# Kernel tuning notes

Hardware: AMD Instinct MI355X
Metric: run time of the kernel (lower is better)

The kernel has to match this reference:

```python
import jax, jax.numpy as jnp
import numpy as np

D, H, COND, MLP_RATIO = 1024, 16, 1024, 4
HD = D // H
DFF = MLP_RATIO * D


def layer_norm(x, w, eps=1e-5):
    xf = x.astype(jnp.float32)
    mu = jnp.mean(xf, axis=-1, keepdims=True)
    var = jnp.mean((xf - mu) ** 2, axis=-1, keepdims=True)
    return (xf - mu) * jax.lax.rsqrt(var + eps) * w


def rms_norm(x, w, eps=1e-6):
    xf = x.astype(jnp.float32)
    rms = jnp.sqrt(jnp.mean(xf * xf, axis=-1, keepdims=True) + eps)
    return (xf / rms * w).astype(x.dtype)


def rotate_half(x):
    x1, x2 = x[..., : x.shape[-1] // 2], x[..., x.shape[-1] // 2:]
    return jnp.concatenate([-x2, x1], axis=-1)


def apply_rope(x, cos, sin):
    return x * cos + rotate_half(x) * sin


def setup_inputs() -> dict:
    key = jax.random.key(0)
    ks = jax.random.split(key, 16)
    B, S = 4, 2048
    pos = jnp.arange(S, dtype=jnp.float32)
    inv = 1.0 / (10000.0 ** (jnp.arange(0, HD, 2, dtype=jnp.float32) / HD))
    freqs = pos[:, None] * inv[None, :]              # (S, HD/2)
    emb = jnp.concatenate([freqs, freqs], axis=-1)   # (S, HD)
    return {
        "x": jax.random.normal(ks[0], (B, S, D), jnp.float32),
        "cos": jnp.cos(emb)[None, :, None, :],        # (1,S,1,HD)
        "sin": jnp.sin(emb)[None, :, None, :],
        "c": jax.random.normal(ks[1], (B, COND), jnp.float32),
        "norm1_w": jnp.ones((D,), jnp.float32),
        "Wqkv": jax.random.normal(ks[2], (D, 3 * D), jnp.float32) * 0.02,
        "Wout": jax.random.normal(ks[3], (D, D), jnp.float32) * 0.02,
        "q_norm_w": jnp.ones((HD,), jnp.float32),
        "k_norm_w": jnp.ones((HD,), jnp.float32),
        "norm2_w": jnp.ones((D,), jnp.float32),
        "W1": jax.random.normal(ks[4], (D, DFF), jnp.float32) * 0.02,
        "b1": jnp.zeros((DFF,), jnp.float32),
        "W2": jax.random.normal(ks[5], (DFF, D), jnp.float32) * 0.02,
        "b2": jnp.zeros((D,), jnp.float32),
        "ada_W": jax.random.normal(ks[6], (COND, 6 * D), jnp.float32) * 0.02,
        "ada_b": jnp.zeros((6 * D,), jnp.float32),
    }


def reference(x, cos, sin, c, norm1_w, Wqkv, Wout, q_norm_w, k_norm_w,
              norm2_w, W1, b1, W2, b2, ada_W, ada_b):
    B, S, _ = x.shape
    mod = (c @ ada_W + ada_b)[:, None, :]            # (B,1,6D)
    sh_msa, sc_msa, g_msa, sh_mlp, sc_mlp, g_mlp = jnp.split(mod, 6, axis=-1)

    x_norm = layer_norm(x, norm1_w) * (1 + sc_msa) + sh_msa
    qkv = (x_norm @ Wqkv).reshape(B, S, 3, H, HD)
    q, k, v = qkv[:, :, 0], qkv[:, :, 1], qkv[:, :, 2]  # (B,S,H,HD)
    q = apply_rope(rms_norm(q, q_norm_w), cos, sin)
    k = apply_rope(rms_norm(k, k_norm_w), cos, sin)

    scale = 1.0 / jnp.sqrt(jnp.float32(HD))
    logits = jnp.einsum('bqhd,bkhd->bhqk', q, k) * scale
    probs = jax.nn.softmax(logits, axis=-1)
    attn = jnp.einsum('bhqk,bkhd->bqhd', probs, v).reshape(B, S, D)

    x = x + g_msa * (attn @ Wout)

    x_norm = layer_norm(x, norm2_w) * (1 + sc_mlp) + sh_mlp
    h = jax.nn.gelu(x_norm @ W1 + b1, approximate=True)
    x = x + g_mlp * (h @ W2 + b2)
    return x
```

## Files before the change

kernel.cpp:

```cpp
#include <hip/hip_runtime.h>
#include <hip/hip_bf16.h>
#include <math.h>

typedef __bf16 bf16;
typedef __bf16 bf16x8 __attribute__((ext_vector_type(8)));
typedef __bf16 bf16x4 __attribute__((ext_vector_type(4)));
typedef float f32x4 __attribute__((ext_vector_type(4)));
typedef short s16x4 __attribute__((ext_vector_type(4)));

#define S_LEN 2048
#define NTOK 8192
#define DIM 1024
#define NH 16
#define HEADD 64
#define DFF 4096
#define MODD 6144

__device__ __forceinline__ float gelu_fast(float x) {
  float u = 0.7978845608028654f * (x + 0.044715f * x * x * x);
  float e = __builtin_amdgcn_exp2f(-2.8853900817779268f * u);
  return x * __builtin_amdgcn_rcpf(1.0f + e);
}

__device__ __forceinline__ void gl_lds16(const bf16* g, bf16* l) {
  __builtin_amdgcn_global_load_lds(
      (const __attribute__((address_space(1))) unsigned int*)g,
      (__attribute__((address_space(3))) unsigned int*)l, 16, 0, 0);
}

__global__ __launch_bounds__(256) void init_mod_kernel(
    const float* __restrict__ ada_b, float* __restrict__ mod) {
  int i = blockIdx.x * 256 + threadIdx.x;
  mod[i] = ada_b[i % MODD];
}

__global__ __launch_bounds__(256) void ada_gemm_kernel(
    const float* __restrict__ cnd, const float* __restrict__ W,
    float* __restrict__ mod) {
  int n = blockIdx.x * 256 + threadIdx.x;
  int k0 = blockIdx.y * 128;
  float a0 = 0.f, a1 = 0.f, a2 = 0.f, a3 = 0.f;
  for (int k = k0; k < k0 + 128; ++k) {
    float w = W[(size_t)k * MODD + n];
    a0 = fmaf(cnd[k], w, a0);
    a1 = fmaf(cnd[1024 + k], w, a1);
    a2 = fmaf(cnd[2048 + k], w, a2);
    a3 = fmaf(cnd[3072 + k], w, a3);
  }
  atomicAdd(&mod[n], a0);
  atomicAdd(&mod[MODD + n], a1);
  atomicAdd(&mod[2 * MODD + n], a2);
  atomicAdd(&mod[3 * MODD + n], a3);
}

__global__ __launch_bounds__(256) void transpose_cast_kernel(
    const float* __restrict__ W, bf16* __restrict__ Wt, int K, int N) {
  __shared__ float tile[32][33];
  int n0 = blockIdx.x * 32, k0 = blockIdx.y * 32;
  int r = threadIdx.x >> 3;
  int c4 = (threadIdx.x & 7) * 4;
  float4 v = *(const float4*)&W[(size_t)(k0 + r) * N + n0 + c4];
  tile[r][c4 + 0] = v.x; tile[r][c4 + 1] = v.y;
  tile[r][c4 + 2] = v.z; tile[r][c4 + 3] = v.w;
  __syncthreads();
  bf16x4 o;
  o[0] = (bf16)tile[c4 + 0][r];
  o[1] = (bf16)tile[c4 + 1][r];
  o[2] = (bf16)tile[c4 + 2][r];
  o[3] = (bf16)tile[c4 + 3][r];
  *(bf16x4*)&Wt[(size_t)(n0 + r) * K + k0 + c4] = o;
}

__global__ __launch_bounds__(256) void vtrans_kernel(
    const bf16* __restrict__ qkv, bf16* __restrict__ VT) {
  __shared__ __align__(16) bf16 t[64][72];
  const int bh = blockIdx.y;
  const int b = bh >> 4, h = bh & 15;
  const int s0 = blockIdx.x * 64;
  const int tid = threadIdx.x;
  {
    const int r = tid >> 2;
    const int c = (tid & 3) * 16;
    const bf16* src =
        qkv + (size_t)(b * S_LEN + s0 + r) * 3072 + 2048 + h * 64 + c;
    *(bf16x8*)&t[r][c] = *(const bf16x8*)src;
    *(bf16x8*)&t[r][c + 8] = *(const bf16x8*)(src + 8);
  }
  __syncthreads();
  {
    const int d = tid & 63;
    const int sc = (tid >> 6) * 16;
    bf16x8 o0, o1;
#pragma unroll
    for (int j = 0; j < 8; ++j) o0[j] = t[sc + j][d];
#pragma unroll
    for (int j = 0; j < 8; ++j) o1[j] = t[sc + 8 + j][d];
    bf16* dst = VT + (size_t)(bh * 64 + d) * S_LEN + s0 + sc;
    *(bf16x8*)dst = o0;
    *(bf16x8*)(dst + 8) = o1;
  }
}

__global__ __launch_bounds__(256) void ln_mod_kernel(
    const float* __restrict__ x, const float* __restrict__ w,
    const float* __restrict__ mod, int sh_off, int sc_off,
    bf16* __restrict__ out) {
  __shared__ float red[8];
  const int row = blockIdx.x;
  const int b = row >> 11;
  const int tid = threadIdx.x;
  const float4 v = ((const float4*)(x + (size_t)row * DIM))[tid];
  float s1 = v.x + v.y + v.z + v.w;
  float s2 = v.x * v.x + v.y * v.y + v.z * v.z + v.w * v.w;
  for (int off = 32; off > 0; off >>= 1) {
    s1 += __shfl_down(s1, off, 64);
    s2 += __shfl_down(s2, off, 64);
  }
  const int wid = tid >> 6;
  if ((tid & 63) == 0) { red[wid] = s1; red[4 + wid] = s2; }
  __syncthreads();
  s1 = red[0] + red[1] + red[2] + red[3];
  s2 = red[4] + red[5] + red[6] + red[7];
  const float mu = s1 * (1.0f / DIM);
  const float inv = rsqrtf(s2 * (1.0f / DIM) - mu * mu + 1e-5f);
  const int c = tid * 4;
  const float* mb = mod + (size_t)b * MODD;
  float xs[4] = {v.x, v.y, v.z, v.w};
  bf16x4 o;
#pragma unroll
  for (int j = 0; j < 4; ++j)
    o[j] = (bf16)(((xs[j] - mu) * inv) * w[c + j] * (1.0f + mb[sc_off + c + j]) +
                  mb[sh_off + c + j]);
  *(bf16x4*)(out + (size_t)row * DIM + c) = o;
}

template <int EPI, int MT, int BN>
__global__ __launch_bounds__(256) void gemm_bt(
    const bf16* __restrict__ A, const bf16* __restrict__ Bt,
    bf16* __restrict__ Cb, float* __restrict__ Cf,
    const float* __restrict__ bias, const float* __restrict__ gmod,
    const float* __restrict__ resid, const float* __restrict__ cosb,
    const float* __restrict__ sinb, const float* __restrict__ qw,
    const float* __restrict__ kw, int M, int N, int K) {
  constexpr int IM = MT / 32;
  constexpr int JN = BN / 32;
  constexpr int AG = MT / 64;
  constexpr int BG = BN / 64;
  __shared__ __align__(16) bf16 As[2][MT * 32];
  __shared__ __align__(16) bf16 Bs[2][BN * 32];
  const int tid = threadIdx.x;
  const int wid = tid >> 6;
  const int lane = tid & 63;
  const int l15 = lane & 15;
  const int quad = lane >> 4;
  const int m0 = blockIdx.y * MT;
  const int n0 = blockIdx.x * BN;
  const int wm = (wid & 1) * (MT / 2);
  const int wn = (wid >> 1) * (BN / 2);

  const int srow = wid * 16 + (lane >> 2);
  const int scol = (lane & 3) * 8;
  const bf16* Ap = A + (size_t)(m0 + srow) * K + scol;
  const bf16* Bp = Bt + (size_t)(n0 + srow) * K + scol;

#pragma unroll
  for (int g = 0; g < AG; ++g)
    gl_lds16(Ap + (size_t)g * 64 * K, As[0] + g * 2048 + wid * 512);
#pragma unroll
  for (int g = 0; g < BG; ++g)
    gl_lds16(Bp + (size_t)g * 64 * K, Bs[0] + g * 2048 + wid * 512);
  __syncthreads();

  f32x4 acc[IM][JN] = {};
  int cur = 0;

  for (int kt = 0; kt < K; kt += 32) {
    if (kt + 32 < K) {
      const int nxt = cur ^ 1;
#pragma unroll
      for (int g = 0; g < AG; ++g)
        gl_lds16(Ap + (size_t)g * 64 * K + kt + 32,
                 As[nxt] + g * 2048 + wid * 512);
#pragma unroll
      for (int g = 0; g < BG; ++g)
        gl_lds16(Bp + (size_t)g * 64 * K + kt + 32,
                 Bs[nxt] + g * 2048 + wid * 512);
    }

    bf16x8 af[IM], bfr[JN];
#pragma unroll
    for (int i = 0; i < IM; ++i)
      af[i] = *(const bf16x8*)&As[cur][(wm + i * 16 + l15) * 32 + quad * 8];
#pragma unroll
    for (int j = 0; j < JN; ++j)
      bfr[j] = *(const bf16x8*)&Bs[cur][(wn + j * 16 + l15) * 32 + quad * 8];
#pragma unroll
    for (int i = 0; i < IM; ++i)
#pragma unroll
      for (int j = 0; j < JN; ++j)
        acc[i][j] = __builtin_amdgcn_mfma_f32_16x16x32_bf16(af[i], bfr[j],
                                                            acc[i][j], 0, 0, 0);

    __syncthreads();
    cur ^= 1;
  }

  if (EPI == 4 && n0 < 2048) {
    const float* nw = ((n0 + wn) < 1024) ? qw : kw;
    float wv[4];
#pragma unroll
    for (int j = 0; j < 4; ++j) wv[j] = nw[j * 16 + l15];
#pragma unroll
    for (int i = 0; i < IM; ++i) {
#pragma unroll
      for (int r = 0; r < 4; ++r) {
        const int m = m0 + wm + i * 16 + quad * 4 + r;
        const int s = m & (S_LEN - 1);
        float v[4];
        float ss = 0.f;
#pragma unroll
        for (int j = 0; j < 4; ++j) { v[j] = acc[i][j][r]; ss += v[j] * v[j]; }
        ss += __shfl_xor(ss, 1, 64);
        ss += __shfl_xor(ss, 2, 64);
        ss += __shfl_xor(ss, 4, 64);
        ss += __shfl_xor(ss, 8, 64);
        const float inv = rsqrtf(ss * (1.0f / HEADD) + 1e-6f);
        float xn[4];
#pragma unroll
        for (int j = 0; j < 4; ++j) xn[j] = v[j] * inv * wv[j];
#pragma unroll
        for (int j = 0; j < 4; ++j) {
          const int d = j * 16 + l15;
          const float rot = (j < 2) ? -xn[j + 2] : xn[j - 2];
          const float o = xn[j] * cosb[s * HEADD + d] + rot * sinb[s * HEADD + d];
          Cb[(size_t)m * N + n0 + wn + d] = (bf16)o;
        }
      }
    }
    return;
  }

#pragma unroll
  for (int i = 0; i < IM; ++i) {
#pragma unroll
    for (int r = 0; r < 4; ++r) {
      const int m = m0 + wm + i * 16 + quad * 4 + r;
#pragma unroll
      for (int j = 0; j < JN; ++j) {
        const int n = n0 + wn + j * 16 + l15;
        float v = acc[i][j][r];
        if (EPI == 0 || EPI == 4) {
          Cb[(size_t)m * N + n] = (bf16)v;
        } else if (EPI == 1) {
          const int b = m >> 11;
          Cf[(size_t)m * N + n] =
              resid[(size_t)m * N + n] + gmod[(size_t)b * MODD + n] * v;
        } else if (EPI == 2) {
          v += bias[n];
          Cb[(size_t)m * N + n] = (bf16)gelu_fast(v);
        } else {
          v += bias[n];
          const int b = m >> 11;
          Cf[(size_t)m * N + n] =
              resid[(size_t)m * N + n] + gmod[(size_t)b * MODD + n] * v;
        }
      }
    }
  }
}

__global__ __launch_bounds__(256) void attn_kernel(
    const bf16* __restrict__ qkv, const bf16* __restrict__ VT,
    bf16* __restrict__ Opart, float* __restrict__ psumbuf) {
  __shared__ __align__(16) bf16 Ks[4096];
  __shared__ __align__(16) bf16 Vs[4096];
  const int flat = blockIdx.x + 16 * (blockIdx.y + 64 * blockIdx.z);
  const int xcd = flat & 7;
  const int idx = flat >> 3;
  const int pair = xcd * 16 + (idx >> 4);
  const int qblk = idx & 15;
  const int bh = pair >> 1;
  const int split = pair & 1;
  const int b = bh >> 4;
  const int h = bh & 15;
  const int q0 = qblk * 128;
  const int tid = threadIdx.x;
  const int wid = tid >> 6;
  const int lane = tid & 63;
  const int l15 = lane & 15;
  const int quad = lane >> 4;

  bf16x8 aq[2][2];
#pragma unroll
  for (int i = 0; i < 2; ++i) {
    const int qrow = q0 + wid * 32 + i * 16 + l15;
    const size_t qbase = (size_t)(b * S_LEN + qrow) * (3 * DIM) + h * HEADD;
    aq[i][0] = *(const bf16x8*)(qkv + qbase + quad * 8);
    aq[i][1] = *(const bf16x8*)(qkv + qbase + 32 + quad * 8);
  }

  const int ksrow = (lane & 32) | ((lane & 4) << 2) | ((lane & 24) >> 1) | (lane & 3);
  const int ksw = ksrow & 7;
  const int vsw = lane & 7;
  const bf16* krow =
      qkv + (size_t)(b * S_LEN + split * 1024 + lane) * 3072 + DIM + h * HEADD;
  const bf16* vrow = VT + (size_t)(bh * 64 + lane) * S_LEN + split * 1024;

  bf16x8 kreg[2], vreg[2];
#pragma unroll
  for (int rr = 0; rr < 2; ++rr) {
    const int ck = wid + 4 * rr;
    kreg[rr] = *(const bf16x8*)(krow + ck * 8);
    vreg[rr] = *(const bf16x8*)(vrow + ck * 8);
  }

  const float cexp = 0.125f * 1.44269504f;
  const bf16 one = (bf16)1.0f;
  const bf16x8 ones8 = {one, one, one, one, one, one, one, one};
  f32x4 oacc[2][4] = {};
  f32x4 psacc[2] = {};

  for (int t = 0; t < 16; ++t) {
    __syncthreads();
#pragma unroll
    for (int rr = 0; rr < 2; ++rr) {
      const int ck = wid + 4 * rr;
      *(bf16x8*)&Ks[ksrow * 64 + ((ck ^ ksw) << 3)] = kreg[rr];
      *(bf16x8*)&Vs[lane * 64 + ((ck ^ vsw) << 3)] = vreg[rr];
    }
    __syncthreads();
    if (t < 15) {
      krow += 64 * 3072;
      vrow += 64;
#pragma unroll
      for (int rr = 0; rr < 2; ++rr) {
        const int ck = wid + 4 * rr;
        kreg[rr] = *(const bf16x8*)(krow + ck * 8);
        vreg[rr] = *(const bf16x8*)(vrow + ck * 8);
      }
    }

    f32x4 sc[2][4] = {};
    __builtin_amdgcn_s_setprio(1);
#pragma unroll
    for (int hh = 0; hh < 2; ++hh) {
#pragma unroll
      for (int cc = 0; cc < 4; ++cc) {
        const int row = cc * 16 + l15;
        const bf16x8 kf =
            *(const bf16x8*)&Ks[row * 64 + (((quad + 4 * hh) ^ (l15 & 7)) << 3)];
#pragma unroll
        for (int i = 0; i < 2; ++i)
          sc[i][cc] = __builtin_amdgcn_mfma_f32_16x16x32_bf16(kf, aq[i][hh],
                                                              sc[i][cc], 0, 0, 0);
      }
    }
    __builtin_amdgcn_s_setprio(0);

    bf16x8 pf[2][2];
#pragma unroll
    for (int i = 0; i < 2; ++i)
#pragma unroll
      for (int c2 = 0; c2 < 2; ++c2) {
        bf16x8 pb;
#pragma unroll
        for (int j = 0; j < 8; ++j) {
          const float p = __builtin_amdgcn_exp2f(
              fmaf(sc[i][2 * c2 + (j >> 2)][j & 3], cexp, -8.0f));
          pb[j] = (bf16)p;
        }
        pf[i][c2] = pb;
      }

    __builtin_amdgcn_s_setprio(1);
#pragma unroll
    for (int i = 0; i < 2; ++i)
#pragma unroll
      for (int c2 = 0; c2 < 2; ++c2)
        psacc[i] = __builtin_amdgcn_mfma_f32_16x16x32_bf16(pf[i][c2], ones8,
                                                           psacc[i], 0, 0, 0);
#pragma unroll
    for (int j = 0; j < 4; ++j) {
      const int d = 16 * j + l15;
      const int drow = d * 64;
      const int dsw = d & 7;
#pragma unroll
      for (int c2 = 0; c2 < 2; ++c2) {
        const bf16x8 vf =
            *(const bf16x8*)&Vs[drow + (((c2 * 4 + quad) ^ dsw) << 3)];
#pragma unroll
        for (int i = 0; i < 2; ++i)
          oacc[i][j] = __builtin_amdgcn_mfma_f32_16x16x32_bf16(pf[i][c2], vf,
                                                               oacc[i][j], 0, 0, 0);
      }
    }
    __builtin_amdgcn_s_setprio(0);
  }

#pragma unroll
  for (int i = 0; i < 2; ++i) {
    if (l15 == 0) {
#pragma unroll
      for (int r = 0; r < 4; ++r) {
        const int qrow = q0 + wid * 32 + i * 16 + quad * 4 + r;
        psumbuf[(size_t)split * (NTOK * NH) +
                (size_t)(b * S_LEN + qrow) * NH + h] = psacc[i][r];
      }
    }
#pragma unroll
    for (int r = 0; r < 4; ++r) {
      const int m = q0 + wid * 32 + i * 16 + quad * 4 + r;
#pragma unroll
      for (int j = 0; j < 4; ++j)
        Opart[(size_t)split * (NTOK * DIM) +
              ((size_t)(b * S_LEN + m) * NH + h) * HEADD + j * 16 + l15] =
            (bf16)oacc[i][j][r];
    }
  }
}

__global__ __launch_bounds__(256) void attn_reduce_kernel(
    const bf16* __restrict__ Opart, const float* __restrict__ psumbuf,
    bf16* __restrict__ attn) {
  const int g = blockIdx.x * 256 + threadIdx.x;
  const int token = g >> 7;
  const int rem = g & 127;
  const int h = rem >> 3;
  const int d0 = (rem & 7) * 8;
  const size_t off = ((size_t)token * NH + h) * HEADD + d0;
  const bf16x8 o0 = *(const bf16x8*)(Opart + off);
  const bf16x8 o1 = *(const bf16x8*)(Opart + (size_t)NTOK * DIM + off);
  const float l = psumbuf[token * NH + h] + psumbuf[NTOK * NH + token * NH + h];
  const float invl = 1.0f / l;
  bf16x8 o;
#pragma unroll
  for (int j = 0; j < 8; ++j)
    o[j] = (bf16)(((float)o0[j] + (float)o1[j]) * invl);
  *(bf16x8*)(attn + off) = o;
}

extern "C" void kernel_launch(void* const* d_in, const int* in_sizes, int n_in,
                              void* d_out, int out_size, void* d_ws,
                              size_t ws_size, hipStream_t stream) {
  const float* x = (const float*)d_in[0];
  const float* cosb = (const float*)d_in[1];
  const float* sinb = (const float*)d_in[2];
  const float* cnd = (const float*)d_in[3];
  const float* norm1_w = (const float*)d_in[4];
  const float* Wqkv = (const float*)d_in[5];
  const float* Wout = (const float*)d_in[6];
  const float* q_norm_w = (const float*)d_in[7];
  const float* k_norm_w = (const float*)d_in[8];
  const float* norm2_w = (const float*)d_in[9];
  const float* W1 = (const float*)d_in[10];
  const float* b1 = (const float*)d_in[11];
  const float* W2 = (const float*)d_in[12];
  const float* b2 = (const float*)d_in[13];
  const float* ada_W = (const float*)d_in[14];
  const float* ada_b = (const float*)d_in[15];
  float* out = (float*)d_out;

  char* p = (char*)d_ws;
  float* mod = (float*)p;   p += (size_t)4 * MODD * 4;
  bf16* WqkvT = (bf16*)p;   p += (size_t)3072 * 1024 * 2;
  bf16* WoutT = (bf16*)p;   p += (size_t)1024 * 1024 * 2;
  bf16* W1T = (bf16*)p;     p += (size_t)4096 * 1024 * 2;
  bf16* W2T = (bf16*)p;     p += (size_t)1024 * 4096 * 2;
  bf16* XN = (bf16*)p;      p += (size_t)NTOK * DIM * 2;
  bf16* QKV = (bf16*)p;     p += (size_t)NTOK * 3 * DIM * 2;
  bf16* ATTN = (bf16*)p;    p += (size_t)NTOK * DIM * 2;
  bf16* Hbuf = (bf16*)p;    p += (size_t)NTOK * DFF * 2;
  bf16* VT = Hbuf;
  bf16* Opart = Hbuf + (size_t)NTOK * DIM;
  float* psumbuf = (float*)(Hbuf + (size_t)3 * NTOK * DIM);

  init_mod_kernel<<<96, 256, 0, stream>>>(ada_b, mod);
  ada_gemm_kernel<<<dim3(24, 8), 256, 0, stream>>>(cnd, ada_W, mod);
  transpose_cast_kernel<<<dim3(96, 32), 256, 0, stream>>>(Wqkv, WqkvT, 1024, 3072);
  transpose_cast_kernel<<<dim3(32, 32), 256, 0, stream>>>(Wout, WoutT, 1024, 1024);
  transpose_cast_kernel<<<dim3(128, 32), 256, 0, stream>>>(W1, W1T, 1024, 4096);
  transpose_cast_kernel<<<dim3(32, 128), 256, 0, stream>>>(W2, W2T, 4096, 1024);
  ln_mod_kernel<<<NTOK, 256, 0, stream>>>(x, norm1_w, mod, 0, 1024, XN);
  gemm_bt<4, 128, 128><<<dim3(24, 64), 256, 0, stream>>>(
      XN, WqkvT, QKV, nullptr, nullptr, nullptr, nullptr, cosb, sinb,
      q_norm_w, k_norm_w, NTOK, 3072, 1024);
  vtrans_kernel<<<dim3(32, 64), 256, 0, stream>>>(QKV, VT);
  attn_kernel<<<dim3(16, 64, 2), 256, 0, stream>>>(QKV, VT, Opart, psumbuf);
  attn_reduce_kernel<<<4096, 256, 0, stream>>>(Opart, psumbuf, ATTN);
  gemm_bt<1, 128, 128><<<dim3(8, 64), 256, 0, stream>>>(
      ATTN, WoutT, nullptr, out, nullptr, mod + 2 * 1024, x, nullptr, nullptr,
      nullptr, nullptr, NTOK, 1024, 1024);
  ln_mod_kernel<<<NTOK, 256, 0, stream>>>(out, norm2_w, mod, 3 * 1024, 4 * 1024, XN);
  gemm_bt<2, 128, 128><<<dim3(32, 64), 256, 0, stream>>>(
      XN, W1T, Hbuf, nullptr, b1, nullptr, nullptr, nullptr, nullptr,
      nullptr, nullptr, NTOK, DFF, 1024);
  gemm_bt<3, 128, 128><<<dim3(8, 64), 256, 0, stream>>>(
      Hbuf, W2T, nullptr, out, b2, mod + 5 * 1024, out, nullptr, nullptr,
      nullptr, nullptr, NTOK, 1024, DFF);
  (void)in_sizes; (void)n_in; (void)out_size; (void)ws_size;
}
```

Measured before the change: 618.2 us.

## Triple-buffer GEMM LDS staging with explicit vmcnt waits and MFMA priority

```diff
diff --git a/kernel.cpp b/kernel.cpp
--- a/kernel.cpp
+++ b/kernel.cpp
@@ -146,8 +146,8 @@
   constexpr int JN = BN / 32;
   constexpr int AG = MT / 64;
   constexpr int BG = BN / 64;
-  __shared__ __align__(16) bf16 As[2][MT * 32];
-  __shared__ __align__(16) bf16 Bs[2][BN * 32];
+  __shared__ __align__(16) bf16 As[3][MT * 32];
+  __shared__ __align__(16) bf16 Bs[3][BN * 32];
   const int tid = threadIdx.x;
   const int wid = tid >> 6;
   const int lane = tid & 63;
@@ -163,29 +163,32 @@
   const bf16* Ap = A + (size_t)(m0 + srow) * K + scol;
   const bf16* Bp = Bt + (size_t)(n0 + srow) * K + scol;
 
-#pragma unroll
-  for (int g = 0; g < AG; ++g)
-    gl_lds16(Ap + (size_t)g * 64 * K, As[0] + g * 2048 + wid * 512);
-#pragma unroll
-  for (int g = 0; g < BG; ++g)
-    gl_lds16(Bp + (size_t)g * 64 * K, Bs[0] + g * 2048 + wid * 512);
-  __syncthreads();
+  auto stage = [&](int buf, int kt) {
+#pragma unroll
+    for (int g = 0; g < AG; ++g)
+      gl_lds16(Ap + (size_t)g * 64 * K + kt, As[buf] + g * 2048 + wid * 512);
+#pragma unroll
+    for (int g = 0; g < BG; ++g)
+      gl_lds16(Bp + (size_t)g * 64 * K + kt, Bs[buf] + g * 2048 + wid * 512);
+  };
+
+  stage(0, 0);
+  stage(1, 32);
 
   f32x4 acc[IM][JN] = {};
-  int cur = 0;
-
-  for (int kt = 0; kt < K; kt += 32) {
-    if (kt + 32 < K) {
-      const int nxt = cur ^ 1;
-#pragma unroll
-      for (int g = 0; g < AG; ++g)
-        gl_lds16(Ap + (size_t)g * 64 * K + kt + 32,
-                 As[nxt] + g * 2048 + wid * 512);
-#pragma unroll
-      for (int g = 0; g < BG; ++g)
-        gl_lds16(Bp + (size_t)g * 64 * K + kt + 32,
-                 Bs[nxt] + g * 2048 + wid * 512);
-    }
+  const int NT = K >> 5;
+  int cur = 0, stg = 2;
+
+  for (int t = 0; t < NT; ++t) {
+    if (t + 2 < NT) {
+      stage(stg, (t + 2) << 5);
+      asm volatile("s_waitcnt vmcnt(8)" ::: "memory");
+    } else if (t + 1 < NT) {
+      asm volatile("s_waitcnt vmcnt(4)" ::: "memory");
+    } else {
+      asm volatile("s_waitcnt vmcnt(0)" ::: "memory");
+    }
+    __builtin_amdgcn_s_barrier();
 
     bf16x8 af[IM], bfr[JN];
 #pragma unroll
@@ -194,15 +197,17 @@
 #pragma unroll
     for (int j = 0; j < JN; ++j)
       bfr[j] = *(const bf16x8*)&Bs[cur][(wn + j * 16 + l15) * 32 + quad * 8];
+    __builtin_amdgcn_s_setprio(1);
 #pragma unroll
     for (int i = 0; i < IM; ++i)
 #pragma unroll
       for (int j = 0; j < JN; ++j)
         acc[i][j] = __builtin_amdgcn_mfma_f32_16x16x32_bf16(af[i], bfr[j],
                                                             acc[i][j], 0, 0, 0);
-
-    __syncthreads();
-    cur ^= 1;
+    __builtin_amdgcn_s_setprio(0);
+    __builtin_amdgcn_s_barrier();
+    cur = (cur == 2) ? 0 : cur + 1;
+    stg = (stg == 2) ? 0 : stg + 1;
   }
 
   if (EPI == 4 && n0 < 2048) {
```

Result: no change. 606.4 us (-1.9%).
